# Performance work log

Hardware: AMD Instinct MI355X
Metric: run time of the kernel (lower is better)

The kernel has to match this reference:

```python
import jax, jax.numpy as jnp
import numpy as np

N_NODES = 100000
N_EDGES = 1600000
IN = 128
OUT = 32
HEADS = 4
NEG_SLOPE = 0.2


def setup_inputs() -> dict:
    key = jax.random.key(0)
    ks = jax.random.split(key, 6)
    x = jax.random.normal(ks[0], (N_NODES, IN), dtype=jnp.float32)
    row = jax.random.randint(ks[1], (N_EDGES,), 0, N_NODES, dtype=jnp.int32)
    col = jax.random.randint(ks[2], (N_EDGES,), 0, N_NODES, dtype=jnp.int32)
    W = jax.random.normal(ks[3], (OUT * HEADS, IN), dtype=jnp.float32) * (1.0 / np.sqrt(IN))
    b = jnp.zeros((OUT * HEADS,), dtype=jnp.float32)
    a_l = jax.random.normal(ks[4], (1, OUT, HEADS), dtype=jnp.float32) * 0.1
    a_r = jax.random.normal(ks[5], (1, OUT, HEADS), dtype=jnp.float32) * 0.1
    return {"x": x, "row": row, "col": col, "W": W, "b": b, "a_l": a_l, "a_r": a_r}


def reference(x, row, col, W, b, a_l, a_r):
    N = x.shape[0]
    # Z: [N, OUT, HEADS] (row-major view of [N, OUT*HEADS], matching torch .view)
    Z = (x @ W.T + b).reshape(N, OUT, HEADS)
    e_l = jnp.sum(Z * a_l, axis=1)  # [N, HEADS]
    e_r = jnp.sum(Z * a_r, axis=1)  # [N, HEADS]
    e = e_l[row] + e_r[col]         # [E, HEADS]
    e = jnp.where(e > 0, e, NEG_SLOPE * e)  # LeakyReLU
    # segment softmax over edges grouped by destination (row)
    m = jax.ops.segment_max(e, row, num_segments=N)      # [N, HEADS]
    ex = jnp.exp(e - m[row])                              # [E, HEADS]
    denom = jax.ops.segment_sum(ex, row, num_segments=N)  # [N, HEADS]
    alpha = ex / denom[row]                               # [E, HEADS]
    # bspmm: out[i,:,h] = sum_{(i,j) in E} alpha[e,h] * Z[j,:,h]
    out = jax.ops.segment_sum(alpha[:, None, :] * Z[col], row, num_segments=N)
    return out
```

## Files before the change

kernel.cpp:

```cpp
#include <hip/hip_runtime.h>
#include <hip/hip_bf16.h>
#include <math.h>


typedef __attribute__((ext_vector_type(8))) short bf16x8;
typedef __attribute__((ext_vector_type(4))) float f32x4;

__device__ __forceinline__ ushort f2bf(float f) {
  __hip_bfloat16 h = __float2bfloat16(f);
  return __builtin_bit_cast(ushort, h);
}
__device__ __forceinline__ float bf2f(ushort u) {
  unsigned v = ((unsigned)u) << 16;
  return __builtin_bit_cast(float, v);
}

__global__ __launch_bounds__(512) void prep0(
    const float* __restrict__ W, ushort* __restrict__ Wh,
    ushort* __restrict__ Wl, int* __restrict__ cntP, int N8) {
  int i = blockIdx.x * 512 + threadIdx.x;
  if (i < 16384) {
    float w = W[i];
    ushort hb = f2bf(w);
    Wh[i] = hb;
    Wl[i] = f2bf(w - bf2f(hb));
  }
  if (i < N8) cntP[i] = 0;
}

__global__ __launch_bounds__(512, 4) void gemm_deg(
    const float* __restrict__ x, const ushort* __restrict__ Wh,
    const ushort* __restrict__ Wl, const float* __restrict__ bias,
    const float* __restrict__ a_l, const float* __restrict__ a_r,
    ushort* __restrict__ Zh, float* __restrict__ el, float* __restrict__ er,
    int N, const int* __restrict__ row, int* __restrict__ cntP,
    int* __restrict__ rank, int E, int G1) {
  __shared__ __align__(16) ushort smem[16896];
  __shared__ float sal[128], sar[128];

  if ((int)blockIdx.x >= G1) {
    int e = ((int)blockIdx.x - G1) * 512 + threadIdx.x;
    if (e < E) {
      int copy = blockIdx.x & 7;
      rank[e] = atomicAdd(&cntP[copy * N + row[e]], 1);
    }
    return;
  }

  const int t = threadIdx.x;
  const int lane = t & 63;
  const int wv = t >> 6;
  const int row0 = blockIdx.x * 128;
  const int l15 = lane & 15, l4 = lane >> 4;
  const int ch = wv * 16 + l15;

  if (t < 128) { sal[t] = a_l[t]; sar[t] = a_r[t]; }

  bf16x8 Bh[4], Bl[4];
#pragma unroll
  for (int kf = 0; kf < 4; ++kf) {
    int off = ch * 128 + kf * 32 + l4 * 8;
    Bh[kf] = *(const bf16x8*)&Wh[off];
    Bl[kf] = *(const bf16x8*)&Wl[off];
  }

  ushort* xh = smem;
#pragma unroll
  for (int i = 0; i < 8; ++i) {
    int f4 = i * 512 + t;
    int r = f4 >> 5;
    int k = (f4 & 31) * 4;
    int gr = row0 + r;
    float4 v = make_float4(0.f, 0.f, 0.f, 0.f);
    if (gr < N) v = ((const float4*)x)[(size_t)gr * 32 + (f4 & 31)];
    int idx = r * 128 + (k ^ ((r & 7) << 3));
    uint2 hv;
    hv.x = f2bf(v.x) | ((unsigned)f2bf(v.y) << 16);
    hv.y = f2bf(v.z) | ((unsigned)f2bf(v.w) << 16);
    *(uint2*)&xh[idx] = hv;
  }
  __syncthreads();

  f32x4 acc[8];
#pragma unroll
  for (int rt = 0; rt < 8; ++rt) acc[rt] = (f32x4){0.f, 0.f, 0.f, 0.f};

#pragma unroll
  for (int kf = 0; kf < 4; ++kf) {
#pragma unroll
    for (int rt = 0; rt < 8; ++rt) {
      int r = rt * 16 + l15;
      int idx = r * 128 + ((kf * 32 + l4 * 8) ^ ((r & 7) << 3));
      bf16x8 ah = *(const bf16x8*)&xh[idx];
      acc[rt] = __builtin_amdgcn_mfma_f32_16x16x32_bf16(ah, Bh[kf], acc[rt], 0, 0, 0);
      acc[rt] = __builtin_amdgcn_mfma_f32_16x16x32_bf16(ah, Bl[kf], acc[rt], 0, 0, 0);
    }
  }
  __syncthreads();

  ushort* zs = smem;
  {
    float bv = bias[ch];
    int o = ch >> 2, h = ch & 3;
    int s = (o & 15) * 8 + h * 2 + (o >> 4);
#pragma unroll
    for (int rt = 0; rt < 8; ++rt) {
#pragma unroll
      for (int j = 0; j < 4; ++j) {
        int r = rt * 16 + l4 * 4 + j;
        zs[r * 132 + s] = f2bf(acc[rt][j] + bv);
      }
    }
  }
  __syncthreads();

  {
    int r = t >> 2;
    int h = t & 3;
    int gr = row0 + r;
    if (gr < N) {
#pragma unroll
      for (int q = 0; q < 4; ++q) {
        uint4 v = *(const uint4*)&zs[r * 132 + h * 32 + q * 8];
        *(uint4*)&Zh[(size_t)gr * 128 + h * 32 + q * 8] = v;
      }
      float sl = 0.f, sr = 0.f;
#pragma unroll
      for (int op = 0; op < 16; ++op) {
        unsigned zz = *(const unsigned*)&zs[r * 132 + op * 8 + h * 2];
        float zlo = bf2f((ushort)(zz & 0xffff));
        float zhi = bf2f((ushort)(zz >> 16));
        int c = (op << 2) + h;
        sl += zlo * sal[c] + zhi * sal[c + 64];
        sr += zlo * sar[c] + zhi * sar[c + 64];
      }
      el[(unsigned)gr * 4 + h] = sl;
      er[(unsigned)gr * 4 + h] = sr;
    }
  }
}

__global__ __launch_bounds__(256) void nscan(
    int* __restrict__ cntP, int* __restrict__ deg, int* __restrict__ base,
    int* __restrict__ bsum, int N) {
  __shared__ int ss[256];
  int t = threadIdx.x;
  int i = blockIdx.x * 256 + t;
  int tot = 0;
  if (i < N) {
    int run = 0;
#pragma unroll
    for (int k = 0; k < 8; ++k) {
      int c = cntP[k * N + i];
      cntP[k * N + i] = run;
      run += c;
    }
    tot = run;
  }
  ss[t] = tot;
  __syncthreads();
#pragma unroll
  for (int off = 1; off < 256; off <<= 1) {
    int u = (t >= off) ? ss[t - off] : 0;
    __syncthreads();
    ss[t] += u;
    __syncthreads();
  }
  if (i < N) {
    base[i] = ss[t] - tot;
    deg[i] = tot;
  }
  if (t == 255) bsum[blockIdx.x] = ss[255];
}

__global__ __launch_bounds__(512) void scan2(int* __restrict__ bsum, int NB) {
  __shared__ int s[512];
  int v = (threadIdx.x < NB) ? bsum[threadIdx.x] : 0;
  s[threadIdx.x] = v;
  __syncthreads();
#pragma unroll
  for (int off = 1; off < 512; off <<= 1) {
    int t = (threadIdx.x >= off) ? s[threadIdx.x - off] : 0;
    __syncthreads();
    s[threadIdx.x] += t;
    __syncthreads();
  }
  if (threadIdx.x < NB) bsum[threadIdx.x] = s[threadIdx.x] - v;
}

__global__ __launch_bounds__(256) void fill(
    const int* __restrict__ row, const int* __restrict__ col,
    const int* __restrict__ rank, const int* __restrict__ base,
    const int* __restrict__ bsum, const int* __restrict__ cntP,
    int* __restrict__ sorted_col, int E, int N, int G1) {
  int e = blockIdx.x * 256 + threadIdx.x;
  if (e >= E) return;
  int r = row[e];
  int copy = (G1 + (e >> 9)) & 7;
  int pos = base[r] + bsum[r >> 8] + cntP[copy * N + r] + rank[e];
  sorted_col[pos] = col[e];
}

__global__ __launch_bounds__(256) void gather(
    const int* __restrict__ base, const int* __restrict__ bsum,
    const int* __restrict__ deg, const int* __restrict__ sorted_col,
    const float* __restrict__ el, const float* __restrict__ er,
    const ushort* __restrict__ Zh, float* __restrict__ out, int N) {
  int t = threadIdx.x;
  int lane = t & 63;
  int n = blockIdx.x * 4 + (t >> 6);
  if (n >= N) return;
  int h = lane & 3;
  int jj = lane >> 2;
  int s = base[n] + bsum[n >> 8];
  int d = deg[n];
  int end = s + d;
  float elv = el[((unsigned)n << 2) + h];
  float acc0 = 0.f, acc1 = 0.f, sumA = 0.f;
  const unsigned* Zh32 = (const unsigned*)Zh;
  const unsigned zlane = (unsigned)lane;
  const int bpb = (lane & 3) << 2;

  for (int p = s; p < end; p += 16) {
    int vn = end - p;
    unsigned pk = 0;
    float xv = 0.f;
    if (jj < vn) {
      int cl = sorted_col[p + jj];
      float e = elv + er[((unsigned)cl << 2) + h];
      e = fmaxf(e, 0.2f * e);
      xv = __expf(e);
      pk = ((unsigned)cl << 15) | (f2bf(xv) & 0x7fffu);
    }
    sumA += xv;
    float xvb[16];
    unsigned addrv[16];
#pragma unroll
    for (int q = 0; q < 16; ++q) {
      int a = bpb + (q << 4);
      unsigned b = (unsigned)__builtin_amdgcn_ds_bpermute(a, (int)pk);
      addrv[q] = ((b >> 15) << 6) + zlane;
      xvb[q] = bf2f((ushort)(b & 0x7fffu));
    }
    unsigned zz[16];
#pragma unroll
    for (int q = 0; q < 16; ++q) zz[q] = Zh32[addrv[q]];
#pragma unroll
    for (int q = 0; q < 16; ++q) {
      acc0 = fmaf(xvb[q], __builtin_bit_cast(float, zz[q] << 16), acc0);
      acc1 = fmaf(xvb[q], __builtin_bit_cast(float, zz[q] & 0xffff0000u), acc1);
    }
  }
  float sum = sumA;
  sum += __shfl_xor(sum, 4, 64);
  sum += __shfl_xor(sum, 8, 64);
  sum += __shfl_xor(sum, 16, 64);
  sum += __shfl_xor(sum, 32, 64);
  float inv = (d > 0) ? 1.0f / sum : 0.f;
  unsigned ob = ((unsigned)n << 7) + zlane;
  __builtin_nontemporal_store(acc0 * inv, &out[ob]);
  __builtin_nontemporal_store(acc1 * inv, &out[ob + 64]);
}

extern "C" void kernel_launch(void* const* d_in, const int* in_sizes, int n_in,
                              void* d_out, int out_size, void* d_ws, size_t ws_size,
                              hipStream_t stream) {
  const float* x   = (const float*)d_in[0];
  const int*   row = (const int*)d_in[1];
  const int*   col = (const int*)d_in[2];
  const float* W   = (const float*)d_in[3];
  const float* b   = (const float*)d_in[4];
  const float* a_l = (const float*)d_in[5];
  const float* a_r = (const float*)d_in[6];
  float* out = (float*)d_out;

  const int N = in_sizes[0] / 128;
  const int E = in_sizes[1];
  const int NB = (N + 255) / 256;

  char* w = (char*)d_ws;
  ushort* Zh       = (ushort*)w;             w += (size_t)N * 128 * 2;
  int*   sorted_col= (int*)w;                w += (size_t)E * 4;
  int*   rank      = (int*)w;                w += (size_t)E * 4;
  float* el        = (float*)w;              w += (size_t)N * 4 * 4;
  float* er        = (float*)w;              w += (size_t)N * 4 * 4;
  int*   cntP      = (int*)w;                w += (size_t)N * 8 * 4;
  int*   deg       = (int*)w;                w += (size_t)N * 4;
  int*   base      = (int*)w;                w += (size_t)N * 4;
  int*   bsum      = (int*)w;                w += 512 * 4;
  ushort* Wh       = (ushort*)w;             w += 16384 * 2;
  ushort* Wl       = (ushort*)w;             w += 16384 * 2;

  const int N8 = N * 8;
  const int P0 = (N8 > 16384 ? N8 : 16384);
  prep0<<<(P0 + 511) / 512, 512, 0, stream>>>(W, Wh, Wl, cntP, N8);

  const int G1 = (N + 127) / 128;
  const int G2 = (E + 511) / 512;
  gemm_deg<<<G1 + G2, 512, 0, stream>>>(x, Wh, Wl, b, a_l, a_r, Zh, el, er,
                                        N, row, cntP, rank, E, G1);

  nscan<<<NB, 256, 0, stream>>>(cntP, deg, base, bsum, N);
  scan2<<<1, 512, 0, stream>>>(bsum, NB);
  fill<<<(E + 255) / 256, 256, 0, stream>>>(row, col, rank, base, bsum, cntP,
                                            sorted_col, E, N, G1);
  gather<<<(N + 3) / 4, 256, 0, stream>>>(base, bsum, deg, sorted_col, el, er,
                                          Zh, out, N);
}
```

Measured before the change: 201.5 us.

## Interleave GEMM tiles with edge-count blocks, drop prep kernel, fold W split inline

Removes the prep0 kernel: W is now split into bf16 hi/lo parts inside each GEMM block, and cntP is zeroed with hipMemsetAsync. Block indices are interleaved so every fifth block is a GEMM tile and the rest do atomic degree counting, which mixes compute-bound and atomic-bound work across the GPU. The fill kernel recomputes the block-to-copy mapping to match the interleaving. gather also gets a min-blocks-per-SM launch bound of 8, which may limit registers per thread.

Result: slower. 211.8 us (+5.1%).

```diff
diff --git a/kernel.cpp b/kernel.cpp
--- a/kernel.cpp
+++ b/kernel.cpp
@@ -15,33 +15,33 @@
   return __builtin_bit_cast(float, v);
 }
 
-__global__ __launch_bounds__(512) void prep0(
-    const float* __restrict__ W, ushort* __restrict__ Wh,
-    ushort* __restrict__ Wl, int* __restrict__ cntP, int N8) {
-  int i = blockIdx.x * 512 + threadIdx.x;
-  if (i < 16384) {
-    float w = W[i];
-    ushort hb = f2bf(w);
-    Wh[i] = hb;
-    Wl[i] = f2bf(w - bf2f(hb));
-  }
-  if (i < N8) cntP[i] = 0;
-}
-
 __global__ __launch_bounds__(512, 4) void gemm_deg(
-    const float* __restrict__ x, const ushort* __restrict__ Wh,
-    const ushort* __restrict__ Wl, const float* __restrict__ bias,
+    const float* __restrict__ x, const float* __restrict__ W,
+    const float* __restrict__ bias,
     const float* __restrict__ a_l, const float* __restrict__ a_r,
     ushort* __restrict__ Zh, float* __restrict__ el, float* __restrict__ er,
     int N, const int* __restrict__ row, int* __restrict__ cntP,
-    int* __restrict__ rank, int E, int G1) {
+    int* __restrict__ rank, int E, int G1, int ilv) {
   __shared__ __align__(16) ushort smem[16896];
   __shared__ float sal[128], sar[128];
 
-  if ((int)blockIdx.x >= G1) {
-    int e = ((int)blockIdx.x - G1) * 512 + threadIdx.x;
+  const int b = (int)blockIdx.x;
+  int tile = -1, tailt = -1;
+  if (ilv) {
+    if ((b % 5 == 0) && (b / 5 < G1)) tile = b / 5;
+    else {
+      int g = (b + 4) / 5;
+      if (g > G1) g = G1;
+      tailt = b - g;
+    }
+  } else {
+    if (b < G1) tile = b; else tailt = b - G1;
+  }
+
+  if (tile < 0) {
+    int e = tailt * 512 + (int)threadIdx.x;
     if (e < E) {
-      int copy = blockIdx.x & 7;
+      int copy = b & 7;
       rank[e] = atomicAdd(&cntP[copy * N + row[e]], 1);
     }
     return;
@@ -50,7 +50,7 @@
   const int t = threadIdx.x;
   const int lane = t & 63;
   const int wv = t >> 6;
-  const int row0 = blockIdx.x * 128;
+  const int row0 = tile * 128;
   const int l15 = lane & 15, l4 = lane >> 4;
   const int ch = wv * 16 + l15;
 
@@ -59,9 +59,19 @@
   bf16x8 Bh[4], Bl[4];
 #pragma unroll
   for (int kf = 0; kf < 4; ++kf) {
-    int off = ch * 128 + kf * 32 + l4 * 8;
-    Bh[kf] = *(const bf16x8*)&Wh[off];
-    Bl[kf] = *(const bf16x8*)&Wl[off];
+    const float* wp = W + (size_t)ch * 128 + kf * 32 + l4 * 8;
+    float4 w0 = *(const float4*)(wp);
+    float4 w1 = *(const float4*)(wp + 4);
+    float wf[8] = {w0.x, w0.y, w0.z, w0.w, w1.x, w1.y, w1.z, w1.w};
+    bf16x8 hi, lo;
+#pragma unroll
+    for (int j = 0; j < 8; ++j) {
+      ushort hb = f2bf(wf[j]);
+      hi[j] = (short)hb;
+      lo[j] = (short)f2bf(wf[j] - bf2f(hb));
+    }
+    Bh[kf] = hi;
+    Bl[kf] = lo;
   }
 
   ushort* xh = smem;
@@ -192,16 +202,19 @@
     const int* __restrict__ row, const int* __restrict__ col,
     const int* __restrict__ rank, const int* __restrict__ base,
     const int* __restrict__ bsum, const int* __restrict__ cntP,
-    int* __restrict__ sorted_col, int E, int N, int G1) {
+    int* __restrict__ sorted_col, int E, int N, int G1, int ilv) {
   int e = blockIdx.x * 256 + threadIdx.x;
   if (e >= E) return;
   int r = row[e];
-  int copy = (G1 + (e >> 9)) & 7;
+  int t9 = e >> 9;
+  int b = ilv ? ((t9 >> 2) * 5 + (t9 & 3) + 1)
+              : (G1 + t9);
+  int copy = b & 7;
   int pos = base[r] + bsum[r >> 8] + cntP[copy * N + r] + rank[e];
   sorted_col[pos] = col[e];
 }
 
-__global__ __launch_bounds__(256) void gather(
+__global__ __launch_bounds__(256, 8) void gather(
     const int* __restrict__ base, const int* __restrict__ bsum,
     const int* __restrict__ deg, const int* __restrict__ sorted_col,
     const float* __restrict__ el, const float* __restrict__ er,
@@ -238,9 +251,9 @@
 #pragma unroll
     for (int q = 0; q < 16; ++q) {
       int a = bpb + (q << 4);
-      unsigned b = (unsigned)__builtin_amdgcn_ds_bpermute(a, (int)pk);
-      addrv[q] = ((b >> 15) << 6) + zlane;
-      xvb[q] = bf2f((ushort)(b & 0x7fffu));
+      unsigned bb = (unsigned)__builtin_amdgcn_ds_bpermute(a, (int)pk);
+      addrv[q] = ((bb >> 15) << 6) + zlane;
+      xvb[q] = bf2f((ushort)(bb & 0x7fffu));
     }
     unsigned zz[16];
 #pragma unroll
@@ -288,22 +301,19 @@
   int*   deg       = (int*)w;                w += (size_t)N * 4;
   int*   base      = (int*)w;                w += (size_t)N * 4;
   int*   bsum      = (int*)w;                w += 512 * 4;
-  ushort* Wh       = (ushort*)w;             w += 16384 * 2;
-  ushort* Wl       = (ushort*)w;             w += 16384 * 2;
-
-  const int N8 = N * 8;
-  const int P0 = (N8 > 16384 ? N8 : 16384);
-  prep0<<<(P0 + 511) / 512, 512, 0, stream>>>(W, Wh, Wl, cntP, N8);
+
+  hipMemsetAsync(cntP, 0, (size_t)N * 8 * sizeof(int), stream);
 
   const int G1 = (N + 127) / 128;
   const int G2 = (E + 511) / 512;
-  gemm_deg<<<G1 + G2, 512, 0, stream>>>(x, Wh, Wl, b, a_l, a_r, Zh, el, er,
-                                        N, row, cntP, rank, E, G1);
+  const int ilv = ((G1 - 1) * 5 < G1 + G2) ? 1 : 0;
+  gemm_deg<<<G1 + G2, 512, 0, stream>>>(x, W, b, a_l, a_r, Zh, el, er,
+                                        N, row, cntP, rank, E, G1, ilv);
 
   nscan<<<NB, 256, 0, stream>>>(cntP, deg, base, bsum, N);
   scan2<<<1, 512, 0, stream>>>(bsum, NB);
   fill<<<(E + 255) / 256, 256, 0, stream>>>(row, col, rank, base, bsum, cntP,
-                                            sorted_col, E, N, G1);
+                                            sorted_col, E, N, G1, ilv);
   gather<<<(N + 3) / 4, 256, 0, stream>>>(base, bsum, deg, sorted_col, el, er,
                                           Zh, out, N);
 }
```
